# Kernel optimization log

Hardware: AMD Instinct MI355X
Metric: run time of the kernel (lower is better)

Reference implementation:

```python
import jax, jax.numpy as jnp
import numpy as np

CODE_DIMS = [256, 512, 1024, 2048]
C = 256
BETA = 0.25
B = 64
N = 1024


def setup_inputs() -> dict:
    key = jax.random.key(0)
    ks = jax.random.split(key, 2 + len(CODE_DIMS))
    z_e = jax.random.normal(ks[0], (B, N, C), dtype=jnp.float32)
    expert_idx = jax.random.randint(ks[1], (B,), 0, len(CODE_DIMS))
    s = 1.0 / np.sqrt(C)  # torch uniform init bound
    inp = {"z_e": z_e, "expert_idx": expert_idx}
    for r, K in enumerate(CODE_DIMS):
        inp[f"cb{r}"] = jax.random.uniform(ks[2 + r], (K, C), minval=-s, maxval=s, dtype=jnp.float32)
    return inp


def _vq_expert(z_e, cb):
    # z_e: [B, N, C], cb: [K, C]
    Bz, Nz, Cz = z_e.shape
    zf = z_e.reshape(-1, Cz)                                  # [B*N, C]
    dists = ((zf ** 2).sum(axis=1, keepdims=True)
             + (cb ** 2).sum(axis=1)[None, :]
             - 2.0 * zf @ cb.T)                               # [B*N, K]
    idx = jnp.argmin(dists, axis=1)                           # [B*N]
    z_q = cb[idx].reshape(Bz, Nz, Cz)                         # [B, N, C]
    return z_q, idx.reshape(Bz, Nz)


def reference(z_e, expert_idx, cb0, cb1, cb2, cb3):
    cbs = [cb0, cb1, cb2, cb3]
    Bz, Nz, Cz = z_e.shape
    sg = jax.lax.stop_gradient
    z_q_out = jnp.zeros_like(z_e)
    indices = jnp.zeros((Bz, Nz), dtype=jnp.int32)
    vq_loss = jnp.asarray(0.0, dtype=z_e.dtype)
    for r, cb in enumerate(cbs):
        z_q, idx = _vq_expert(z_e, cb)
        mask = expert_idx == r                                # [B]
        mf = mask.astype(z_e.dtype)[:, None, None]            # [B,1,1]
        cnt = mask.sum().astype(z_e.dtype)
        denom = jnp.maximum(cnt * Nz * Cz, 1.0)               # mean over masked subset
        codebook_loss = jnp.sum(mf * (sg(z_q) - z_e) ** 2) / denom
        commit_loss = jnp.sum(mf * (z_q - sg(z_e)) ** 2) / denom
        loss_r = (codebook_loss + BETA * commit_loss) / Cz
        frac = cnt / Bz                                       # z_in.numel()/z_e.numel()
        vq_loss = vq_loss + frac * loss_r
        z_q_st = z_e + sg(z_q - z_e)                          # straight-through
        z_q_out = jnp.where(mf > 0, z_q_st, z_q_out)
        indices = jnp.where(mask[:, None], idx.astype(jnp.int32), indices)
    return z_q_out, indices, vq_loss
```

## Files before the change

kernel.cpp:

```cpp
#include <hip/hip_runtime.h>
#include <hip/hip_bf16.h>


#define EPS_GAP 2e-3f
#define NTOK 65536

#define STR 40

typedef __attribute__((ext_vector_type(8))) short bf16x8;
typedef __attribute__((ext_vector_type(4))) float f32x4;

__device__ inline unsigned short f2bf(float f) {
  __hip_bfloat16 h = __float2bfloat16(f);
  unsigned short u;
  __builtin_memcpy(&u, &h, 2);
  return u;
}
__device__ inline float bf2f(unsigned short u) {
  return __uint_as_float(((unsigned)u) << 16);
}

__global__ __launch_bounds__(256) void csum_split_kernel(
    const float* __restrict__ cb0, const float* __restrict__ cb1,
    const float* __restrict__ cb2, const float* __restrict__ cb3,
    float* __restrict__ csums, double* __restrict__ csums64,
    unsigned short* __restrict__ cb_hi, unsigned short* __restrict__ cb_lo,
    int* __restrict__ wl_cnt) {
  if (blockIdx.x == 0 && threadIdx.x == 0) wl_cnt[0] = 0;
  int row = blockIdx.x * 4 + (threadIdx.x >> 6);
  int lane = threadIdx.x & 63;
  const float* src; int r;
  if (row < 256)       { src = cb0; r = row; }
  else if (row < 768)  { src = cb1; r = row - 256; }
  else if (row < 1792) { src = cb2; r = row - 768; }
  else                 { src = cb3; r = row - 1792; }
  float4 v = ((const float4*)(src + r * 256))[lane];
  unsigned short h0 = f2bf(v.x), h1 = f2bf(v.y), h2 = f2bf(v.z), h3 = f2bf(v.w);
  unsigned short l0 = f2bf(v.x - bf2f(h0)), l1 = f2bf(v.y - bf2f(h1));
  unsigned short l2 = f2bf(v.z - bf2f(h2)), l3 = f2bf(v.w - bf2f(h3));
  *(ushort4*)(cb_hi + (size_t)row * 256 + lane * 4) = make_ushort4(h0, h1, h2, h3);
  *(ushort4*)(cb_lo + (size_t)row * 256 + lane * 4) = make_ushort4(l0, l1, l2, l3);
  double s = (double)v.x*v.x + (double)v.y*v.y + (double)v.z*v.z + (double)v.w*v.w;
  #pragma unroll
  for (int off = 32; off >= 1; off >>= 1) s += __shfl_down(s, off, 64);
  if (lane == 0) { csums[row] = (float)s; csums64[row] = s; }
}

__global__ __launch_bounds__(256) void zsq_kernel(const float* __restrict__ z,
                                                  double* __restrict__ parts) {
  const float4* p = (const float4*)z;
  const int n4 = 4194304;
  double s = 0.0;
  for (int i = blockIdx.x * 256 + threadIdx.x; i < n4; i += 256 * 256) {
    float4 v = p[i];
    s += (double)v.x*(double)v.x + (double)v.y*(double)v.y
       + (double)v.z*(double)v.z + (double)v.w*(double)v.w;
  }
  #pragma unroll
  for (int off = 32; off >= 1; off >>= 1) s += __shfl_down(s, off, 64);
  __shared__ double sh[4];
  if ((threadIdx.x & 63) == 0) sh[threadIdx.x >> 6] = s;
  __syncthreads();
  if (threadIdx.x == 0) parts[blockIdx.x] = sh[0] + sh[1] + sh[2] + sh[3];
}

__global__ __launch_bounds__(512, 4) void vq_mfma(
    const float* __restrict__ z_e, const int* __restrict__ expert_idx,
    const unsigned short* __restrict__ cb_hi, const unsigned short* __restrict__ cb_lo,
    const float* __restrict__ csums,
    float* __restrict__ D1, int* __restrict__ K1, float* __restrict__ D2) {
  const int b  = blockIdx.y;
  const int e  = expert_idx[b];
  const int hc = blockIdx.z;
  if (hc >= (2 << e)) return;
  const int cs_off = (e == 0) ? 0 : (e == 1) ? 256 : (e == 2) ? 768 : 1792;
  const int krow0  = cs_off + hc * 128;
  const int t0     = b * 1024 + blockIdx.x * 128;

  __shared__ ushort smem[4 * 128 * STR];
  __shared__ float  sh_cs[128];
  ushort* Ah = smem;
  ushort* Al = smem + 128 * STR;
  ushort* Bh = smem + 2 * 128 * STR;
  ushort* Bl = smem + 3 * 128 * STR;

  const int tid = threadIdx.x;
  if (tid < 128) sh_cs[tid] = csums[krow0 + tid];

  const int w = tid >> 6, l = tid & 63;
  const int h = w >> 2, q = w & 3;
  const int m16 = l & 15, g = l >> 4;

  f32x4 acc[4][2];
  #pragma unroll
  for (int i = 0; i < 4; ++i)
    #pragma unroll
    for (int j = 0; j < 2; ++j) acc[i][j] = (f32x4){0.f, 0.f, 0.f, 0.f};

  for (int kp = 0; kp < 8; ++kp) {
    const int kc = kp * 32;
    __syncthreads();
    #pragma unroll
    for (int it = 0; it < 2; ++it) {
      int idx = tid + it * 512;
      int row = idx >> 3, seg = idx & 7;
      float4 v = *(const float4*)(z_e + (size_t)(t0 + row) * 256 + kc + seg * 4);
      unsigned short h0 = f2bf(v.x), h1 = f2bf(v.y), h2 = f2bf(v.z), h3 = f2bf(v.w);
      unsigned short q0 = f2bf(v.x - bf2f(h0)), q1 = f2bf(v.y - bf2f(h1));
      unsigned short q2 = f2bf(v.z - bf2f(h2)), q3 = f2bf(v.w - bf2f(h3));
      *(ushort4*)(Ah + row * STR + seg * 4) = make_ushort4(h0, h1, h2, h3);
      *(ushort4*)(Al + row * STR + seg * 4) = make_ushort4(q0, q1, q2, q3);
    }
    {
      int row = tid >> 2, seg = tid & 3;
      const size_t go = (size_t)(krow0 + row) * 256 + kc + seg * 8;
      *(float4*)(Bh + row * STR + seg * 8) = *(const float4*)(cb_hi + go);
      *(float4*)(Bl + row * STR + seg * 8) = *(const float4*)(cb_lo + go);
    }
    __syncthreads();
    bf16x8 bh[2], bl[2];
    #pragma unroll
    for (int j = 0; j < 2; ++j) {
      int n = (q * 32 + j * 16 + m16) * STR + g * 8;
      bh[j] = *(bf16x8*)(Bh + n);
      bl[j] = *(bf16x8*)(Bl + n);
    }
    #pragma unroll
    for (int i = 0; i < 4; ++i) {
      int a = (h * 64 + i * 16 + m16) * STR + g * 8;
      bf16x8 ah = *(bf16x8*)(Ah + a);
      bf16x8 al = *(bf16x8*)(Al + a);
      #pragma unroll
      for (int j = 0; j < 2; ++j) {
        acc[i][j] = __builtin_amdgcn_mfma_f32_16x16x32_bf16(ah, bh[j], acc[i][j], 0, 0, 0);
        acc[i][j] = __builtin_amdgcn_mfma_f32_16x16x32_bf16(al, bh[j], acc[i][j], 0, 0, 0);
        acc[i][j] = __builtin_amdgcn_mfma_f32_16x16x32_bf16(ah, bl[j], acc[i][j], 0, 0, 0);
      }
    }
  }

  __syncthreads();
  float* mD = (float*)smem;
  int*   mK = (int*)(smem + 1024);
  float* mS = (float*)(smem + 2048);

  #pragma unroll
  for (int i = 0; i < 4; ++i) {
    #pragma unroll
    for (int r = 0; r < 4; ++r) {
      int k0 = q * 32 + m16;
      float d0 = sh_cs[k0]      - 2.0f * acc[i][0][r];
      float d1 = sh_cs[k0 + 16] - 2.0f * acc[i][1][r];
      float bv, sv; int bk;
      if (d0 <= d1) { bv = d0; bk = k0; sv = d1; }
      else          { bv = d1; bk = k0 + 16; sv = d0; }
      #pragma unroll
      for (int off = 8; off >= 1; off >>= 1) {
        float ov = __shfl_xor(bv, off);
        int   ok = __shfl_xor(bk, off);
        float os = __shfl_xor(sv, off);
        float nb; int nk;
        if (ov < bv || (ov == bv && ok < bk)) { nb = ov; nk = ok; }
        else                                  { nb = bv; nk = bk; }
        sv = fminf(fmaxf(bv, ov), fminf(sv, os));
        bv = nb; bk = nk;
      }
      if (m16 == 0) {
        int tloc = h * 64 + i * 16 + g * 4 + r;
        mD[tloc * 4 + q] = bv;
        mK[tloc * 4 + q] = bk;
        mS[tloc * 4 + q] = sv;
      }
    }
  }
  __syncthreads();
  if (tid < 128) {
    float B = 3.4e38f, S = 3.4e38f; int Kb = 0;
    #pragma unroll
    for (int c = 0; c < 4; ++c) {
      float d1v = mD[tid * 4 + c];
      int   k1v = mK[tid * 4 + c];
      float d2v = mS[tid * 4 + c];
      S = fminf(fmaxf(B, d1v), fminf(S, d2v));
      if (d1v < B) { B = d1v; Kb = k1v; }
    }
    int tg = t0 + tid;
    D1[hc * NTOK + tg] = B;
    K1[hc * NTOK + tg] = hc * 128 + Kb;
    D2[hc * NTOK + tg] = S;
  }
}

__global__ __launch_bounds__(256) void combine_kernel(
    const int* __restrict__ expert_idx,
    const float* __restrict__ D1, const int* __restrict__ K1,
    const float* __restrict__ D2,
    float* __restrict__ idx_out, unsigned char* __restrict__ flags,
    double* __restrict__ parts) {
  const int t = blockIdx.x * 256 + threadIdx.x;
  const int e = expert_idx[t >> 10];
  const int nch = 2 << e;
  float B = 3.4e38f, S = 3.4e38f; int Kb = 0;
  for (int c = 0; c < nch; ++c) {
    float d1 = D1[c * NTOK + t];
    int   k1 = K1[c * NTOK + t];
    float d2 = D2[c * NTOK + t];
    S = fminf(fmaxf(B, d1), fminf(S, d2));
    if (d1 < B) { B = d1; Kb = k1; }
  }
  idx_out[t] = (float)Kb;
  flags[t] = (S - B < EPS_GAP) ? 1 : 0;
  double s = (double)B;
  #pragma unroll
  for (int off = 32; off >= 1; off >>= 1) s += __shfl_down(s, off, 64);
  __shared__ double sh[4];
  if ((threadIdx.x & 63) == 0) sh[threadIdx.x >> 6] = s;
  __syncthreads();
  if (threadIdx.x == 0) parts[blockIdx.x] = sh[0] + sh[1] + sh[2] + sh[3];
}

__global__ __launch_bounds__(256) void compact_kernel(
    const unsigned char* __restrict__ flags,
    int* __restrict__ wl, int* __restrict__ wl_cnt) {
  const int t = blockIdx.x * 256 + threadIdx.x;
  if (flags[t]) {
    int p = atomicAdd(wl_cnt, 1);
    wl[p] = t;
  }
}

__global__ __launch_bounds__(256) void zq_gather_kernel(
    const int* __restrict__ expert_idx,
    const float* __restrict__ cb0, const float* __restrict__ cb1,
    const float* __restrict__ cb2, const float* __restrict__ cb3,
    const float* __restrict__ idx_out, float* __restrict__ zq_out) {
  const int tok  = blockIdx.x * 4 + (threadIdx.x >> 6);
  const int lane = threadIdx.x & 63;
  const int e = expert_idx[tok >> 10];
  const float* cb = (e == 0) ? cb0 : (e == 1) ? cb1 : (e == 2) ? cb2 : cb3;
  const int row = (int)idx_out[tok];
  ((float4*)(zq_out + (size_t)tok * 256))[lane] =
      ((const float4*)(cb + (size_t)row * 256))[lane];
}

__global__ __launch_bounds__(256) void rescue_kernel(
    const float* __restrict__ z_e, const int* __restrict__ expert_idx,
    const float* __restrict__ cb0, const float* __restrict__ cb1,
    const float* __restrict__ cb2, const float* __restrict__ cb3,
    const double* __restrict__ csums64,
    const int* __restrict__ wl, const int* __restrict__ wl_cnt,
    float* __restrict__ zq_out, float* __restrict__ idx_out) {
  __shared__ float  szrow[256];
  __shared__ double szs[4];
  __shared__ float  sdv[3][256];
  __shared__ int    skv[3][256];
  __shared__ int    s_kc;
  const int tid = threadIdx.x;
  const int wid = tid >> 6, lane = tid & 63;
  const int n = wl_cnt[0];
  for (int it = blockIdx.x; it < n; it += gridDim.x) {
    const int t = wl[it];
    const int b = t >> 10;
    const int e = expert_idx[b];
    const int K = 256 << e;
    const float* cb = (e == 0) ? cb0 : (e == 1) ? cb1 : (e == 2) ? cb2 : cb3;
    const int off = (e == 0) ? 0 : (e == 1) ? 256 : (e == 2) ? 768 : 1792;
    const double* cs64 = csums64 + off;

    __syncthreads();
    float zv = z_e[(size_t)t * 256 + tid];
    szrow[tid] = zv;
    double zsq = (double)zv * (double)zv;
    #pragma unroll
    for (int o = 32; o >= 1; o >>= 1) zsq += __shfl_down(zsq, o, 64);
    if (lane == 0) szs[wid] = zsq;
    __syncthreads();
    const float zs_mid = (float)(szs[0] + szs[1] + szs[2] + szs[3]);
    const unsigned zu = __float_as_uint(zs_mid);
    float zs[3] = {__uint_as_float(zu - 1), zs_mid, __uint_as_float(zu + 1)};

    float bd[3] = {3.4e38f, 3.4e38f, 3.4e38f};
    int   bk[3] = {1 << 30, 1 << 30, 1 << 30};
    const float4* z4 = (const float4*)szrow;
    for (int k = tid; k < K; k += 256) {
      const float4* c4 = (const float4*)(cb + (size_t)k * 256);
      double d0 = 0.0, d1v = 0.0, d2v = 0.0, d3 = 0.0;
      for (int qq = 0; qq < 64; qq += 4) {
        float4 a0 = z4[qq],     c0 = c4[qq];
        float4 a1 = z4[qq + 1], c1 = c4[qq + 1];
        float4 a2 = z4[qq + 2], c2 = c4[qq + 2];
        float4 a3 = z4[qq + 3], c3 = c4[qq + 3];
        d0 += (double)a0.x*c0.x + (double)a0.y*c0.y + (double)a0.z*c0.z + (double)a0.w*c0.w;
        d1v+= (double)a1.x*c1.x + (double)a1.y*c1.y + (double)a1.z*c1.z + (double)a1.w*c1.w;
        d2v+= (double)a2.x*c2.x + (double)a2.y*c2.y + (double)a2.z*c2.z + (double)a2.w*c2.w;
        d3 += (double)a3.x*c3.x + (double)a3.y*c3.y + (double)a3.z*c3.z + (double)a3.w*c3.w;
      }
      double dot = (d0 + d1v) + (d2v + d3);
      const float c32 = (float)cs64[k];
      const float m2d = (float)(2.0 * dot);
      #pragma unroll
      for (int v = 0; v < 3; ++v) {
        float T1  = zs[v] + c32;
        float d32 = T1 - m2d;
        if (d32 < bd[v]) { bd[v] = d32; bk[v] = k; }
      }
    }
    #pragma unroll
    for (int v = 0; v < 3; ++v) { sdv[v][tid] = bd[v]; skv[v][tid] = bk[v]; }
    __syncthreads();
    for (int s = 128; s >= 1; s >>= 1) {
      if (tid < s) {
        #pragma unroll
        for (int v = 0; v < 3; ++v) {
          float od = sdv[v][tid + s]; int ok = skv[v][tid + s];
          if (od < sdv[v][tid] || (od == sdv[v][tid] && ok < skv[v][tid])) {
            sdv[v][tid] = od; skv[v][tid] = ok;
          }
        }
      }
      __syncthreads();
    }
    if (tid == 0) {
      int k0 = skv[0][0], k1 = skv[1][0], k2 = skv[2][0];
      int kc = (k0 == k2) ? k0 : k1;
      s_kc = kc;
      idx_out[t] = (float)kc;
    }
    __syncthreads();
    const int kc = s_kc;
    if (tid < 64)
      ((float4*)(zq_out + (size_t)t * 256))[tid] =
          ((const float4*)(cb + (size_t)kc * 256))[tid];
  }
}

__global__ __launch_bounds__(256) void finalize_kernel(const double* __restrict__ parts,
                                                       float* __restrict__ loss_out) {
  double s = parts[threadIdx.x] + parts[threadIdx.x + 256];
  #pragma unroll
  for (int off = 32; off >= 1; off >>= 1) s += __shfl_down(s, off, 64);
  __shared__ double sh[4];
  if ((threadIdx.x & 63) == 0) sh[threadIdx.x >> 6] = s;
  __syncthreads();
  if (threadIdx.x == 0)
    loss_out[0] = (float)((sh[0] + sh[1] + sh[2] + sh[3]) * (1.25 / 4294967296.0));
}

extern "C" void kernel_launch(void* const* d_in, const int* in_sizes, int n_in,
                              void* d_out, int out_size, void* d_ws, size_t ws_size,
                              hipStream_t stream) {
  const float* z_e  = (const float*)d_in[0];
  const int*   eidx = (const int*)d_in[1];
  const float* cb0  = (const float*)d_in[2];
  const float* cb1  = (const float*)d_in[3];
  const float* cb2  = (const float*)d_in[4];
  const float* cb3  = (const float*)d_in[5];

  float* zq    = (float*)d_out;
  float* idxf  = (float*)d_out + 16777216;
  float* lossf = (float*)d_out + 16777216 + 65536;

  char* wsp = (char*)d_ws;
  double*         parts_comb = (double*)wsp;           wsp += 256 * 8;
  double*         parts_zsq  = (double*)wsp;           wsp += 256 * 8;
  double*         csums64    = (double*)wsp;           wsp += 3840 * 8;
  float*          csums      = (float*)wsp;            wsp += 3840 * 4;
  int*            wl_cnt     = (int*)wsp;              wsp += 16;
  unsigned char*  flags      = (unsigned char*)wsp;    wsp += NTOK;
  int*            wl         = (int*)wsp;              wsp += NTOK * 4;
  unsigned short* cb_hi      = (unsigned short*)wsp;   wsp += 3840 * 256 * 2;
  unsigned short* cb_lo      = (unsigned short*)wsp;   wsp += 3840 * 256 * 2;
  float*          D1         = (float*)wsp;            wsp += 16 * NTOK * 4;
  int*            K1         = (int*)wsp;              wsp += 16 * NTOK * 4;
  float*          D2         = (float*)wsp;            wsp += 16 * NTOK * 4;

  csum_split_kernel<<<960, 256, 0, stream>>>(cb0, cb1, cb2, cb3,
                                             csums, csums64, cb_hi, cb_lo, wl_cnt);
  zsq_kernel<<<256, 256, 0, stream>>>(z_e, parts_zsq);
  dim3 grid(8, 64, 16);
  vq_mfma<<<grid, 512, 0, stream>>>(z_e, eidx, cb_hi, cb_lo, csums, D1, K1, D2);
  combine_kernel<<<256, 256, 0, stream>>>(eidx, D1, K1, D2, idxf, flags, parts_comb);
  compact_kernel<<<256, 256, 0, stream>>>(flags, wl, wl_cnt);
  zq_gather_kernel<<<16384, 256, 0, stream>>>(eidx, cb0, cb1, cb2, cb3, idxf, zq);
  rescue_kernel<<<2048, 256, 0, stream>>>(z_e, eidx, cb0, cb1, cb2, cb3,
                                          csums64, wl, wl_cnt, zq, idxf);
  finalize_kernel<<<1, 256, 0, stream>>>(parts_comb, lossf);
}
```

Measured before the change: 481.3 us.

## Swizzle LDS tiles, use direct global-to-LDS loads, fuse compaction into combine

Replaces the padded LDS layout in the MFMA distance kernel with an XOR-swizzled 32-wide layout. Codebook tiles are loaded via global_load_lds, and z is converted with packed bf16 instructions; launch bounds are raised for higher occupancy. The separate compact kernel is merged into combine using atomics directly, and the zsq reduction uses more blocks, with finalize now summing the zsq partials. Occupancy pressure on registers and atomic contention are the main risks.

New measurement: 425.7 us. 11.6% less time.

```diff
diff --git a/kernel.cpp b/kernel.cpp
--- a/kernel.cpp
+++ b/kernel.cpp
@@ -4,8 +4,6 @@
 
 #define EPS_GAP 2e-3f
 #define NTOK 65536
-
-#define STR 40
 
 typedef __attribute__((ext_vector_type(8))) short bf16x8;
 typedef __attribute__((ext_vector_type(4))) float f32x4;
@@ -18,6 +16,12 @@
 }
 __device__ inline float bf2f(unsigned short u) {
   return __uint_as_float(((unsigned)u) << 16);
+}
+
+__device__ inline void gll16(const unsigned short* g, unsigned short* l) {
+  __builtin_amdgcn_global_load_lds(
+      (const __attribute__((address_space(1))) unsigned int*)g,
+      (__attribute__((address_space(3))) unsigned int*)l, 16, 0, 0);
 }
 
 __global__ __launch_bounds__(256) void csum_split_kernel(
@@ -51,7 +55,7 @@
   const float4* p = (const float4*)z;
   const int n4 = 4194304;
   double s = 0.0;
-  for (int i = blockIdx.x * 256 + threadIdx.x; i < n4; i += 256 * 256) {
+  for (int i = blockIdx.x * 256 + threadIdx.x; i < n4; i += 256 * 1024) {
     float4 v = p[i];
     s += (double)v.x*(double)v.x + (double)v.y*(double)v.y
        + (double)v.z*(double)v.z + (double)v.w*(double)v.w;
@@ -64,7 +68,7 @@
   if (threadIdx.x == 0) parts[blockIdx.x] = sh[0] + sh[1] + sh[2] + sh[3];
 }
 
-__global__ __launch_bounds__(512, 4) void vq_mfma(
+__global__ __launch_bounds__(512, 8) void vq_mfma(
     const float* __restrict__ z_e, const int* __restrict__ expert_idx,
     const unsigned short* __restrict__ cb_hi, const unsigned short* __restrict__ cb_lo,
     const float* __restrict__ csums,
@@ -77,12 +81,12 @@
   const int krow0  = cs_off + hc * 128;
   const int t0     = b * 1024 + blockIdx.x * 128;
 
-  __shared__ ushort smem[4 * 128 * STR];
+  __shared__ unsigned short smem[4 * 128 * 32];
   __shared__ float  sh_cs[128];
-  ushort* Ah = smem;
-  ushort* Al = smem + 128 * STR;
-  ushort* Bh = smem + 2 * 128 * STR;
-  ushort* Bl = smem + 3 * 128 * STR;
+  unsigned short* Ah = smem;
+  unsigned short* Al = smem + 128 * 32;
+  unsigned short* Bh = smem + 2 * 128 * 32;
+  unsigned short* Bl = smem + 3 * 128 * 32;
 
   const int tid = threadIdx.x;
   if (tid < 128) sh_cs[tid] = csums[krow0 + tid];
@@ -91,6 +95,12 @@
   const int h = w >> 2, q = w & 3;
   const int m16 = l & 15, g = l >> 4;
 
+  const int brow   = w * 16 + (l >> 2);
+  const int bchunk = (l & 3) ^ ((brow >> 1) & 3);
+  const size_t bsrc0 = (size_t)(krow0 + brow) * 256 + (size_t)bchunk * 8;
+  unsigned short* bh_dst = Bh + w * 512;
+  unsigned short* bl_dst = Bl + w * 512;
+
   f32x4 acc[4][2];
   #pragma unroll
   for (int i = 0; i < 4; ++i)
@@ -100,34 +110,39 @@
   for (int kp = 0; kp < 8; ++kp) {
     const int kc = kp * 32;
     __syncthreads();
+    gll16(cb_hi + bsrc0 + kc, bh_dst);
+    gll16(cb_lo + bsrc0 + kc, bl_dst);
     #pragma unroll
     for (int it = 0; it < 2; ++it) {
       int idx = tid + it * 512;
       int row = idx >> 3, seg = idx & 7;
       float4 v = *(const float4*)(z_e + (size_t)(t0 + row) * 256 + kc + seg * 4);
-      unsigned short h0 = f2bf(v.x), h1 = f2bf(v.y), h2 = f2bf(v.z), h3 = f2bf(v.w);
-      unsigned short q0 = f2bf(v.x - bf2f(h0)), q1 = f2bf(v.y - bf2f(h1));
-      unsigned short q2 = f2bf(v.z - bf2f(h2)), q3 = f2bf(v.w - bf2f(h3));
-      *(ushort4*)(Ah + row * STR + seg * 4) = make_ushort4(h0, h1, h2, h3);
-      *(ushort4*)(Al + row * STR + seg * 4) = make_ushort4(q0, q1, q2, q3);
-    }
-    {
-      int row = tid >> 2, seg = tid & 3;
-      const size_t go = (size_t)(krow0 + row) * 256 + kc + seg * 8;
-      *(float4*)(Bh + row * STR + seg * 8) = *(const float4*)(cb_hi + go);
-      *(float4*)(Bl + row * STR + seg * 8) = *(const float4*)(cb_lo + go);
+      unsigned hxy, hzw, lxy, lzw;
+      asm("v_cvt_pk_bf16_f32 %0, %1, %2" : "=v"(hxy) : "v"(v.x), "v"(v.y));
+      asm("v_cvt_pk_bf16_f32 %0, %1, %2" : "=v"(hzw) : "v"(v.z), "v"(v.w));
+      float lx = v.x - __uint_as_float(hxy << 16);
+      float ly = v.y - __uint_as_float(hxy & 0xffff0000u);
+      float lz = v.z - __uint_as_float(hzw << 16);
+      float lw = v.w - __uint_as_float(hzw & 0xffff0000u);
+      asm("v_cvt_pk_bf16_f32 %0, %1, %2" : "=v"(lxy) : "v"(lx), "v"(ly));
+      asm("v_cvt_pk_bf16_f32 %0, %1, %2" : "=v"(lzw) : "v"(lz), "v"(lw));
+      int off = row * 32 + ((((seg >> 1) ^ ((row >> 1) & 3)) << 3) | ((seg & 1) << 2));
+      *(uint2*)(Ah + off) = make_uint2(hxy, hzw);
+      *(uint2*)(Al + off) = make_uint2(lxy, lzw);
     }
     __syncthreads();
     bf16x8 bh[2], bl[2];
     #pragma unroll
     for (int j = 0; j < 2; ++j) {
-      int n = (q * 32 + j * 16 + m16) * STR + g * 8;
+      int r = q * 32 + j * 16 + m16;
+      int n = r * 32 + ((g ^ ((r >> 1) & 3)) << 3);
       bh[j] = *(bf16x8*)(Bh + n);
       bl[j] = *(bf16x8*)(Bl + n);
     }
     #pragma unroll
     for (int i = 0; i < 4; ++i) {
-      int a = (h * 64 + i * 16 + m16) * STR + g * 8;
+      int r = h * 64 + i * 16 + m16;
+      int a = r * 32 + ((g ^ ((r >> 1) & 3)) << 3);
       bf16x8 ah = *(bf16x8*)(Ah + a);
       bf16x8 al = *(bf16x8*)(Al + a);
       #pragma unroll
@@ -195,7 +210,8 @@
     const int* __restrict__ expert_idx,
     const float* __restrict__ D1, const int* __restrict__ K1,
     const float* __restrict__ D2,
-    float* __restrict__ idx_out, unsigned char* __restrict__ flags,
+    float* __restrict__ idx_out,
+    int* __restrict__ wl, int* __restrict__ wl_cnt,
     double* __restrict__ parts) {
   const int t = blockIdx.x * 256 + threadIdx.x;
   const int e = expert_idx[t >> 10];
@@ -209,7 +225,10 @@
     if (d1 < B) { B = d1; Kb = k1; }
   }
   idx_out[t] = (float)Kb;
-  flags[t] = (S - B < EPS_GAP) ? 1 : 0;
+  if (S - B < EPS_GAP) {
+    int p = atomicAdd(wl_cnt, 1);
+    wl[p] = t;
+  }
   double s = (double)B;
   #pragma unroll
   for (int off = 32; off >= 1; off >>= 1) s += __shfl_down(s, off, 64);
@@ -217,16 +236,6 @@
   if ((threadIdx.x & 63) == 0) sh[threadIdx.x >> 6] = s;
   __syncthreads();
   if (threadIdx.x == 0) parts[blockIdx.x] = sh[0] + sh[1] + sh[2] + sh[3];
-}
-
-__global__ __launch_bounds__(256) void compact_kernel(
-    const unsigned char* __restrict__ flags,
-    int* __restrict__ wl, int* __restrict__ wl_cnt) {
-  const int t = blockIdx.x * 256 + threadIdx.x;
-  if (flags[t]) {
-    int p = atomicAdd(wl_cnt, 1);
-    wl[p] = t;
-  }
 }
 
 __global__ __launch_bounds__(256) void zq_gather_kernel(
@@ -334,15 +343,18 @@
   }
 }
 
-__global__ __launch_bounds__(256) void finalize_kernel(const double* __restrict__ parts,
-                                                       float* __restrict__ loss_out) {
-  double s = parts[threadIdx.x] + parts[threadIdx.x + 256];
+__global__ __launch_bounds__(256) void finalize_kernel(
+    const double* __restrict__ parts_comb, const double* __restrict__ parts_zsq,
+    float* __restrict__ loss_out) {
+  const int tid = threadIdx.x;
+  double s = parts_comb[tid] + parts_zsq[tid] + parts_zsq[tid + 256]
+           + parts_zsq[tid + 512] + parts_zsq[tid + 768];
   #pragma unroll
   for (int off = 32; off >= 1; off >>= 1) s += __shfl_down(s, off, 64);
   __shared__ double sh[4];
-  if ((threadIdx.x & 63) == 0) sh[threadIdx.x >> 6] = s;
-  __syncthreads();
-  if (threadIdx.x == 0)
+  if ((tid & 63) == 0) sh[tid >> 6] = s;
+  __syncthreads();
+  if (tid == 0)
     loss_out[0] = (float)((sh[0] + sh[1] + sh[2] + sh[3]) * (1.25 / 4294967296.0));
 }
 
@@ -362,11 +374,10 @@
 
   char* wsp = (char*)d_ws;
   double*         parts_comb = (double*)wsp;           wsp += 256 * 8;
-  double*         parts_zsq  = (double*)wsp;           wsp += 256 * 8;
+  double*         parts_zsq  = (double*)wsp;           wsp += 1024 * 8;
   double*         csums64    = (double*)wsp;           wsp += 3840 * 8;
   float*          csums      = (float*)wsp;            wsp += 3840 * 4;
   int*            wl_cnt     = (int*)wsp;              wsp += 16;
-  unsigned char*  flags      = (unsigned char*)wsp;    wsp += NTOK;
   int*            wl         = (int*)wsp;              wsp += NTOK * 4;
   unsigned short* cb_hi      = (unsigned short*)wsp;   wsp += 3840 * 256 * 2;
   unsigned short* cb_lo      = (unsigned short*)wsp;   wsp += 3840 * 256 * 2;
@@ -376,13 +387,12 @@
 
   csum_split_kernel<<<960, 256, 0, stream>>>(cb0, cb1, cb2, cb3,
                                              csums, csums64, cb_hi, cb_lo, wl_cnt);
-  zsq_kernel<<<256, 256, 0, stream>>>(z_e, parts_zsq);
+  zsq_kernel<<<1024, 256, 0, stream>>>(z_e, parts_zsq);
   dim3 grid(8, 64, 16);
   vq_mfma<<<grid, 512, 0, stream>>>(z_e, eidx, cb_hi, cb_lo, csums, D1, K1, D2);
-  combine_kernel<<<256, 256, 0, stream>>>(eidx, D1, K1, D2, idxf, flags, parts_comb);
-  compact_kernel<<<256, 256, 0, stream>>>(flags, wl, wl_cnt);
+  combine_kernel<<<256, 256, 0, stream>>>(eidx, D1, K1, D2, idxf, wl, wl_cnt, parts_comb);
   zq_gather_kernel<<<16384, 256, 0, stream>>>(eidx, cb0, cb1, cb2, cb3, idxf, zq);
   rescue_kernel<<<2048, 256, 0, stream>>>(z_e, eidx, cb0, cb1, cb2, cb3,
                                           csums64, wl, wl_cnt, zq, idxf);
-  finalize_kernel<<<1, 256, 0, stream>>>(parts_comb, lossf);
-}
+  finalize_kernel<<<1, 256, 0, stream>>>(parts_comb, parts_zsq, lossf);
+}
```
